# Kernel optimization log

Measured on AMD Instinct MI355X. Metric: run time of the kernel, lower is better.

Reference implementation:

```python
import jax, jax.numpy as jnp
import numpy as np

N_NODES = 50000
N_EDGES = 800000
FEAT = 128
HID1 = 128
HID2 = 64


def setup_inputs() -> dict:
    key = jax.random.key(0)
    k = jax.random.split(key, 6)
    x = jax.random.normal(k[0], (N_NODES, FEAT), dtype=jnp.float32)
    edge_index = jax.random.randint(k[1], (2, N_EDGES), 0, N_NODES, dtype=jnp.int32)
    # Glorot-style init scaling like PyG's GCNConv linear
    W1 = jax.random.normal(k[2], (FEAT, HID1), dtype=jnp.float32) * (1.0 / np.sqrt(FEAT))
    b1 = jnp.zeros((HID1,), dtype=jnp.float32)
    W2 = jax.random.normal(k[3], (HID1, HID2), dtype=jnp.float32) * (1.0 / np.sqrt(HID1))
    b2 = jnp.zeros((HID2,), dtype=jnp.float32)
    return {"x": x, "edge_index": edge_index, "W1": W1, "b1": b1, "W2": W2, "b2": b2}


def _gcn_conv(x, src, dst, W, b, n_nodes):
    """PyG GCNConv: h = X W; out_i = sum_j norm_ij h_j + b, with self-loops and
    symmetric normalization norm_ij = deg_i^-1/2 * deg_j^-1/2 (deg counts self-loop)."""
    h = x @ W  # [N, out]
    # degree at target nodes (self-loops already appended to src/dst)
    deg = jax.ops.segment_sum(jnp.ones_like(dst, dtype=h.dtype), dst, num_segments=n_nodes)
    dinv = jax.lax.rsqrt(jnp.maximum(deg, 1.0))  # deg >= 1 because of self-loops
    norm = dinv[src] * dinv[dst]  # [E+N]
    msg = h[src] * norm[:, None]  # gather + scale, [E+N, out]
    out = jax.ops.segment_sum(msg, dst, num_segments=n_nodes)
    return out + b


def reference(x, edge_index, W1, b1, W2, b2):
    n = x.shape[0]
    self_idx = jnp.arange(n, dtype=edge_index.dtype)
    src = jnp.concatenate([edge_index[0], self_idx])
    dst = jnp.concatenate([edge_index[1], self_idx])
    h = jax.nn.relu(_gcn_conv(x, src, dst, W1, b1, n))
    out = _gcn_conv(h, src, dst, W2, b2, n)
    return out
```

## Files before the change

### kernel.cpp

```cpp
#include <hip/hip_runtime.h>
#include <hip/hip_bf16.h>


#define POISON 0xAAAAAAAAu

typedef __attribute__((ext_vector_type(8))) short short8;
typedef __attribute__((ext_vector_type(4))) float f32x4;

__device__ __forceinline__ float bf_lo(unsigned u) { return __uint_as_float(u << 16); }
__device__ __forceinline__ float bf_hi(unsigned u) { return __uint_as_float(u & 0xffff0000u); }
__device__ __forceinline__ unsigned short f2bf(float f) {
    return (unsigned short)(__bfloat16_as_ushort(__float2bfloat16(f)));
}

__global__ __launch_bounds__(256) void countpack_kernel(
    const int* __restrict__ dst, unsigned* __restrict__ ucnt,
    int* __restrict__ eslot, int E,
    const float* __restrict__ W1, unsigned short* __restrict__ Wp1,
    const float* __restrict__ W2, unsigned short* __restrict__ Wp2) {
    constexpr int PB = (128 * 128 + 128 * 64) / 256;
    if ((int)blockIdx.x < PB) {
        int q = blockIdx.x * 256 + threadIdx.x;
        if (q < 128 * 128) {
            int j = q & 7;
            int n = (q >> 3) & 127;
            int kb = q >> 10;
            Wp1[q] = f2bf(W1[(kb * 8 + j) * 128 + n]);
        } else {
            int p = q - 128 * 128;
            int j = p & 7;
            int n = (p >> 3) & 63;
            int kb = p >> 9;
            Wp2[p] = f2bf(W2[(kb * 8 + j) * 64 + n]);
        }
        return;
    }
    int e = (blockIdx.x - PB) * 256 + threadIdx.x;
    if (e < E) eslot[e] = (int)(atomicAdd(&ucnt[dst[e]], 1u) - POISON);
}

__global__ __launch_bounds__(256) void alloc_kernel(unsigned* __restrict__ ucnt,
                                                    int* __restrict__ row_ptr,
                                                    float* __restrict__ dinv, int N) {
    int i = blockIdx.x * 256 + threadIdx.x;
    int lane = threadIdx.x & 63;
    int c = (i < N) ? (int)(ucnt[i] - POISON) : 0;
    if (i < N) dinv[i] = rsqrtf((float)(c + 1));
    int incl = c;
#pragma unroll
    for (int off = 1; off < 64; off <<= 1) {
        int u = __shfl_up(incl, off, 64);
        if (lane >= off) incl += u;
    }
    int base = 0;
    if (lane == 63) base = (int)(atomicAdd(&ucnt[N], (unsigned)incl) - POISON);
    base = __shfl(base, 63, 64);
    if (i < N) row_ptr[i] = base + incl - c;
}

__global__ __launch_bounds__(256) void scatgemm_kernel(
    const int* __restrict__ src, const int* __restrict__ dst,
    const int* __restrict__ row_ptr, const int* __restrict__ eslot,
    int* __restrict__ ssrc, int E,
    const float* __restrict__ X, const unsigned short* __restrict__ Wp1,
    const float* __restrict__ dinv, unsigned short* __restrict__ g1,
    int N, int gb) {
    if ((int)blockIdx.x >= gb) {
        int e0 = (blockIdx.x - gb) * 1024 + threadIdx.x * 4;
        if (e0 + 3 < E) {
            int4 d4 = *(const int4*)(dst + e0);
            int4 s4 = *(const int4*)(src + e0);
            int4 t4 = *(const int4*)(eslot + e0);
            ssrc[row_ptr[d4.x] + t4.x] = s4.x;
            ssrc[row_ptr[d4.y] + t4.y] = s4.y;
            ssrc[row_ptr[d4.z] + t4.z] = s4.z;
            ssrc[row_ptr[d4.w] + t4.w] = s4.w;
        } else {
            for (int e = e0; e < E; ++e)
                ssrc[row_ptr[dst[e]] + eslot[e]] = src[e];
        }
        return;
    }
    constexpr int NT = 8;
    const int lane = threadIdx.x & 63;
    const int wave = threadIdx.x >> 6;
    const int col = lane & 15;
    const int quad = lane >> 4;
    const int row0w = (blockIdx.x * 4 + wave) * 16;

    int arow = row0w + col;
    if (arow >= N) arow = N - 1;

    short8 afr[4];
    const float* Xr = X + (size_t)arow * 128;
#pragma unroll
    for (int c = 0; c < 4; ++c) {
        float4 f0 = *(const float4*)(Xr + c * 32 + quad * 8);
        float4 f1 = *(const float4*)(Xr + c * 32 + quad * 8 + 4);
        short8 a;
        a[0] = (short)f2bf(f0.x); a[1] = (short)f2bf(f0.y);
        a[2] = (short)f2bf(f0.z); a[3] = (short)f2bf(f0.w);
        a[4] = (short)f2bf(f1.x); a[5] = (short)f2bf(f1.y);
        a[6] = (short)f2bf(f1.z); a[7] = (short)f2bf(f1.w);
        afr[c] = a;
    }

    f32x4 acc[NT];
#pragma unroll
    for (int t = 0; t < NT; ++t) acc[t] = (f32x4){0.f, 0.f, 0.f, 0.f};

    const uint4* Wq = (const uint4*)Wp1;
#pragma unroll
    for (int c = 0; c < 4; ++c) {
        short8 bfr[NT];
#pragma unroll
        for (int t = 0; t < NT; ++t) {
            union { uint4 u; short8 s; } cv;
            cv.u = Wq[(size_t)(c * 4 + quad) * 128 + t * 16 + col];
            bfr[t] = cv.s;
        }
#pragma unroll
        for (int t = 0; t < NT; ++t)
            acc[t] = __builtin_amdgcn_mfma_f32_16x16x32_bf16(afr[c], bfr[t], acc[t], 0, 0, 0);
    }

#pragma unroll
    for (int r = 0; r < 4; ++r) {
        int row = row0w + quad * 4 + r;
        if (row < N) {
            float dv = dinv[row];
#pragma unroll
            for (int t = 0; t < NT; ++t)
                g1[(size_t)row * 128 + t * 16 + col] = f2bf(acc[t][r] * dv);
        }
    }
}

__global__ __launch_bounds__(256) void aggmm_kernel(const unsigned short* __restrict__ g1,
                                                    const int* __restrict__ row_ptr,
                                                    const unsigned* __restrict__ ucnt,
                                                    const int* __restrict__ ssrc,
                                                    const float* __restrict__ dinv,
                                                    const float* __restrict__ b1,
                                                    const unsigned short* __restrict__ Wp2,
                                                    unsigned short* __restrict__ g2, int N) {
    __shared__ unsigned short zt[16][136];
    __shared__ float sdinv[16];
    const int lane = threadIdx.x & 63;
    const int wave = threadIdx.x >> 6;
    const int nodebase = blockIdx.x * 16;
    const unsigned* hp = (const unsigned*)g1;

    const float bx = b1[2 * lane];
    const float by = b1[2 * lane + 1];

#pragma unroll
    for (int k = 0; k < 4; ++k) {
        int zr = wave * 4 + k;
        int node = __builtin_amdgcn_readfirstlane(nodebase + zr);
        unsigned pk = 0;
        if (node < N) {
            float di = dinv[node];
            int beg = row_ptr[node];
            int end = beg + (int)(ucnt[node] - POISON);
            unsigned hv = hp[node * 64 + lane];
            float ax0 = bf_lo(hv), ay0 = bf_hi(hv);
            float ax1 = 0.f, ay1 = 0.f;
            int j = beg;
            for (; j + 7 < end; j += 8) {
                int s0 = ssrc[j + 0], s1 = ssrc[j + 1], s2 = ssrc[j + 2], s3 = ssrc[j + 3];
                int s4 = ssrc[j + 4], s5 = ssrc[j + 5], s6 = ssrc[j + 6], s7 = ssrc[j + 7];
                unsigned v0 = hp[s0 * 64 + lane], v1 = hp[s1 * 64 + lane];
                unsigned v2 = hp[s2 * 64 + lane], v3 = hp[s3 * 64 + lane];
                unsigned v4 = hp[s4 * 64 + lane], v5 = hp[s5 * 64 + lane];
                unsigned v6 = hp[s6 * 64 + lane], v7 = hp[s7 * 64 + lane];
                ax0 += bf_lo(v0) + bf_lo(v1) + bf_lo(v2) + bf_lo(v3);
                ax1 += bf_lo(v4) + bf_lo(v5) + bf_lo(v6) + bf_lo(v7);
                ay0 += bf_hi(v0) + bf_hi(v1) + bf_hi(v2) + bf_hi(v3);
                ay1 += bf_hi(v4) + bf_hi(v5) + bf_hi(v6) + bf_hi(v7);
            }
            for (; j + 3 < end; j += 4) {
                int s0 = ssrc[j + 0], s1 = ssrc[j + 1], s2 = ssrc[j + 2], s3 = ssrc[j + 3];
                unsigned v0 = hp[s0 * 64 + lane], v1 = hp[s1 * 64 + lane];
                unsigned v2 = hp[s2 * 64 + lane], v3 = hp[s3 * 64 + lane];
                ax0 += bf_lo(v0) + bf_lo(v1);
                ax1 += bf_lo(v2) + bf_lo(v3);
                ay0 += bf_hi(v0) + bf_hi(v1);
                ay1 += bf_hi(v2) + bf_hi(v3);
            }
            for (; j < end; ++j) {
                unsigned v = hp[ssrc[j] * 64 + lane];
                ax0 += bf_lo(v);
                ay0 += bf_hi(v);
            }
            float ax = fmaxf((ax0 + ax1) * di + bx, 0.f);
            float ay = fmaxf((ay0 + ay1) * di + by, 0.f);
            pk = (unsigned)f2bf(ax) | ((unsigned)f2bf(ay) << 16);
            if (lane == 0) sdinv[zr] = di;
        } else if (lane == 0) {
            sdinv[zr] = 0.f;
        }
        ((unsigned*)&zt[zr][0])[lane] = pk;
    }
    __syncthreads();

    const int col = lane & 15;
    const int quad = lane >> 4;
    short8 afr[4];
#pragma unroll
    for (int c = 0; c < 4; ++c) {
        union { uint4 u; short8 s; } cv;
        cv.u = *(const uint4*)&zt[col][c * 32 + quad * 8];
        afr[c] = cv.s;
    }
    f32x4 acc = (f32x4){0.f, 0.f, 0.f, 0.f};
    const uint4* Wq = (const uint4*)Wp2;
#pragma unroll
    for (int c = 0; c < 4; ++c) {
        union { uint4 u; short8 s; } cv;
        cv.u = Wq[(size_t)(c * 4 + quad) * 64 + wave * 16 + col];
        acc = __builtin_amdgcn_mfma_f32_16x16x32_bf16(afr[c], cv.s, acc, 0, 0, 0);
    }
#pragma unroll
    for (int r = 0; r < 4; ++r) {
        int row = nodebase + quad * 4 + r;
        if (row < N)
            g2[(size_t)row * 64 + wave * 16 + col] = f2bf(acc[r] * sdinv[quad * 4 + r]);
    }
}

__global__ __launch_bounds__(256) void agg2_kernel(const unsigned short* __restrict__ g,
                                                   const int* __restrict__ row_ptr,
                                                   const unsigned* __restrict__ ucnt,
                                                   const int* __restrict__ ssrc,
                                                   const float* __restrict__ dinv,
                                                   const float* __restrict__ bias,
                                                   float* __restrict__ out, int N) {
    int node = __builtin_amdgcn_readfirstlane((int)(blockIdx.x * 4 + (threadIdx.x >> 6)));
    if (node >= N) return;
    int lane = threadIdx.x & 63;
    float di = dinv[node];
    int beg = row_ptr[node];
    int end = beg + (int)(ucnt[node] - POISON);

    float a0 = __uint_as_float((unsigned)g[node * 64 + lane] << 16);
    float a1 = 0.f;
    int j = beg;
    for (; j + 7 < end; j += 8) {
        int s0 = ssrc[j + 0], s1 = ssrc[j + 1], s2 = ssrc[j + 2], s3 = ssrc[j + 3];
        int s4 = ssrc[j + 4], s5 = ssrc[j + 5], s6 = ssrc[j + 6], s7 = ssrc[j + 7];
        float v0 = __uint_as_float((unsigned)g[s0 * 64 + lane] << 16);
        float v1 = __uint_as_float((unsigned)g[s1 * 64 + lane] << 16);
        float v2 = __uint_as_float((unsigned)g[s2 * 64 + lane] << 16);
        float v3 = __uint_as_float((unsigned)g[s3 * 64 + lane] << 16);
        float v4 = __uint_as_float((unsigned)g[s4 * 64 + lane] << 16);
        float v5 = __uint_as_float((unsigned)g[s5 * 64 + lane] << 16);
        float v6 = __uint_as_float((unsigned)g[s6 * 64 + lane] << 16);
        float v7 = __uint_as_float((unsigned)g[s7 * 64 + lane] << 16);
        a0 += v0 + v1 + v2 + v3;
        a1 += v4 + v5 + v6 + v7;
    }
    for (; j + 3 < end; j += 4) {
        int s0 = ssrc[j + 0], s1 = ssrc[j + 1], s2 = ssrc[j + 2], s3 = ssrc[j + 3];
        float v0 = __uint_as_float((unsigned)g[s0 * 64 + lane] << 16);
        float v1 = __uint_as_float((unsigned)g[s1 * 64 + lane] << 16);
        float v2 = __uint_as_float((unsigned)g[s2 * 64 + lane] << 16);
        float v3 = __uint_as_float((unsigned)g[s3 * 64 + lane] << 16);
        a0 += v0 + v1;
        a1 += v2 + v3;
    }
    for (; j < end; ++j)
        a0 += __uint_as_float((unsigned)g[ssrc[j] * 64 + lane] << 16);
    out[node * 64 + lane] = (a0 + a1) * di + bias[lane];
}

extern "C" void kernel_launch(void* const* d_in, const int* in_sizes, int n_in,
                              void* d_out, int out_size, void* d_ws, size_t ws_size,
                              hipStream_t stream) {
    const float* x = (const float*)d_in[0];
    const int* eidx = (const int*)d_in[1];
    const float* W1 = (const float*)d_in[2];
    const float* b1 = (const float*)d_in[3];
    const float* W2 = (const float*)d_in[4];
    const float* b2 = (const float*)d_in[5];
    float* out = (float*)d_out;

    const int N = in_sizes[0] / 128;
    const int E = in_sizes[1] / 2;
    const int* src = eidx;
    const int* dst = eidx + E;

    char* ws = (char*)d_ws;
    size_t off = 0;
    auto alloc = [&](size_t bytes) -> char* {
        char* p = ws + off;
        off = (off + bytes + 255) & ~(size_t)255;
        return p;
    };
    unsigned* ucnt = (unsigned*)alloc((size_t)(N + 1) * 4);
    int* row_ptr = (int*)alloc((size_t)N * 4);
    int* eslot = (int*)alloc((size_t)E * 4);
    int* ssrc = (int*)alloc((size_t)E * 4);
    float* dinv = (float*)alloc((size_t)N * 4);
    unsigned short* Wp1 = (unsigned short*)alloc(128 * 128 * 2);
    unsigned short* Wp2 = (unsigned short*)alloc(128 * 64 * 2);
    unsigned short* g1 = (unsigned short*)alloc((size_t)N * 128 * 2);
    unsigned short* g2 = (unsigned short*)alloc((size_t)N * 64 * 2);

    const int nbN = (N + 255) / 256;
    const int nbE = (E + 255) / 256;
    const int nbE4 = (E + 1023) / 1024;
    const int gb = (N + 63) / 64;
    constexpr int PB = (128 * 128 + 128 * 64) / 256;

    countpack_kernel<<<PB + nbE, 256, 0, stream>>>(dst, ucnt, eslot, E, W1, Wp1, W2, Wp2);
    alloc_kernel<<<nbN, 256, 0, stream>>>(ucnt, row_ptr, dinv, N);
    scatgemm_kernel<<<gb + nbE4, 256, 0, stream>>>(src, dst, row_ptr, eslot, ssrc, E,
                                                   x, Wp1, dinv, g1, N, gb);
    aggmm_kernel<<<(N + 15) / 16, 256, 0, stream>>>(g1, row_ptr, ucnt, ssrc, dinv, b1, Wp2, g2, N);
    agg2_kernel<<<(N + 3) / 4, 256, 0, stream>>>(g2, row_ptr, ucnt, ssrc, dinv, b2, out, N);
}
```

Measured before the change: 196.3 us.

## Split wave into half-wave node gathers with 8-byte loads and vectorize degree counting

The layer-1 aggregation now gives each half-wave (32 lanes) its own node, and every lane gathers 8 bytes (four bf16 features) per neighbor instead of 4. Two nodes are processed in parallel per wave, which is meant to raise memory-level parallelism on the irregular gather and cut per-node loop overhead. The degree-counting kernel now handles four edges per thread with int4 loads and stores, using a quarter of the blocks. In exchange, the aggregation unroll drops from 8 to 4, and the two half-waves can diverge when their nodes have different degrees.

```diff
diff --git a/kernel.cpp b/kernel.cpp
--- a/kernel.cpp
+++ b/kernel.cpp
@@ -35,8 +35,19 @@
         }
         return;
     }
-    int e = (blockIdx.x - PB) * 256 + threadIdx.x;
-    if (e < E) eslot[e] = (int)(atomicAdd(&ucnt[dst[e]], 1u) - POISON);
+    int e0 = (blockIdx.x - PB) * 1024 + threadIdx.x * 4;
+    if (e0 + 3 < E) {
+        int4 d4 = *(const int4*)(dst + e0);
+        int4 t;
+        t.x = (int)(atomicAdd(&ucnt[d4.x], 1u) - POISON);
+        t.y = (int)(atomicAdd(&ucnt[d4.y], 1u) - POISON);
+        t.z = (int)(atomicAdd(&ucnt[d4.z], 1u) - POISON);
+        t.w = (int)(atomicAdd(&ucnt[d4.w], 1u) - POISON);
+        *(int4*)(eslot + e0) = t;
+    } else {
+        for (int e = e0; e < E; ++e)
+            eslot[e] = (int)(atomicAdd(&ucnt[dst[e]], 1u) - POISON);
+    }
 }
 
 __global__ __launch_bounds__(256) void alloc_kernel(unsigned* __restrict__ ucnt,
@@ -148,59 +159,60 @@
     __shared__ float sdinv[16];
     const int lane = threadIdx.x & 63;
     const int wave = threadIdx.x >> 6;
+    const int h = lane >> 5;
+    const int u = lane & 31;
     const int nodebase = blockIdx.x * 16;
-    const unsigned* hp = (const unsigned*)g1;
-
-    const float bx = b1[2 * lane];
-    const float by = b1[2 * lane + 1];
-
-#pragma unroll
-    for (int k = 0; k < 4; ++k) {
-        int zr = wave * 4 + k;
-        int node = __builtin_amdgcn_readfirstlane(nodebase + zr);
-        unsigned pk = 0;
-        if (node < N) {
-            float di = dinv[node];
-            int beg = row_ptr[node];
-            int end = beg + (int)(ucnt[node] - POISON);
-            unsigned hv = hp[node * 64 + lane];
-            float ax0 = bf_lo(hv), ay0 = bf_hi(hv);
-            float ax1 = 0.f, ay1 = 0.f;
-            int j = beg;
-            for (; j + 7 < end; j += 8) {
-                int s0 = ssrc[j + 0], s1 = ssrc[j + 1], s2 = ssrc[j + 2], s3 = ssrc[j + 3];
-                int s4 = ssrc[j + 4], s5 = ssrc[j + 5], s6 = ssrc[j + 6], s7 = ssrc[j + 7];
-                unsigned v0 = hp[s0 * 64 + lane], v1 = hp[s1 * 64 + lane];
-                unsigned v2 = hp[s2 * 64 + lane], v3 = hp[s3 * 64 + lane];
-                unsigned v4 = hp[s4 * 64 + lane], v5 = hp[s5 * 64 + lane];
-                unsigned v6 = hp[s6 * 64 + lane], v7 = hp[s7 * 64 + lane];
-                ax0 += bf_lo(v0) + bf_lo(v1) + bf_lo(v2) + bf_lo(v3);
-                ax1 += bf_lo(v4) + bf_lo(v5) + bf_lo(v6) + bf_lo(v7);
-                ay0 += bf_hi(v0) + bf_hi(v1) + bf_hi(v2) + bf_hi(v3);
-                ay1 += bf_hi(v4) + bf_hi(v5) + bf_hi(v6) + bf_hi(v7);
-            }
-            for (; j + 3 < end; j += 4) {
-                int s0 = ssrc[j + 0], s1 = ssrc[j + 1], s2 = ssrc[j + 2], s3 = ssrc[j + 3];
-                unsigned v0 = hp[s0 * 64 + lane], v1 = hp[s1 * 64 + lane];
-                unsigned v2 = hp[s2 * 64 + lane], v3 = hp[s3 * 64 + lane];
-                ax0 += bf_lo(v0) + bf_lo(v1);
-                ax1 += bf_lo(v2) + bf_lo(v3);
-                ay0 += bf_hi(v0) + bf_hi(v1);
-                ay1 += bf_hi(v2) + bf_hi(v3);
-            }
-            for (; j < end; ++j) {
-                unsigned v = hp[ssrc[j] * 64 + lane];
-                ax0 += bf_lo(v);
-                ay0 += bf_hi(v);
-            }
-            float ax = fmaxf((ax0 + ax1) * di + bx, 0.f);
-            float ay = fmaxf((ay0 + ay1) * di + by, 0.f);
-            pk = (unsigned)f2bf(ax) | ((unsigned)f2bf(ay) << 16);
-            if (lane == 0) sdinv[zr] = di;
-        } else if (lane == 0) {
-            sdinv[zr] = 0.f;
-        }
-        ((unsigned*)&zt[zr][0])[lane] = pk;
+    const uint2* hp2 = (const uint2*)g1;
+
+    const float4 b4 = *(const float4*)(b1 + 4 * u);
+
+#pragma unroll
+    for (int k = 0; k < 2; ++k) {
+        int zr = wave * 4 + k * 2 + h;
+        int node = nodebase + zr;
+        bool act = node < N;
+        float di = 0.f;
+        int beg = 0, deg = 0;
+        uint2 hv = {0u, 0u};
+        if (act) {
+            di = dinv[node];
+            beg = row_ptr[node];
+            deg = (int)(ucnt[node] - POISON);
+            hv = hp2[(size_t)node * 32 + u];
+        }
+        float a0 = 0.f, a1 = 0.f, a2 = 0.f, a3 = 0.f;
+        int j = 0;
+        for (; j + 4 <= deg; j += 4) {
+            int s0 = ssrc[beg + j + 0], s1 = ssrc[beg + j + 1];
+            int s2 = ssrc[beg + j + 2], s3 = ssrc[beg + j + 3];
+            uint2 v0 = hp2[(size_t)s0 * 32 + u];
+            uint2 v1 = hp2[(size_t)s1 * 32 + u];
+            uint2 v2 = hp2[(size_t)s2 * 32 + u];
+            uint2 v3 = hp2[(size_t)s3 * 32 + u];
+            a0 += bf_lo(v0.x) + bf_lo(v1.x) + bf_lo(v2.x) + bf_lo(v3.x);
+            a1 += bf_hi(v0.x) + bf_hi(v1.x) + bf_hi(v2.x) + bf_hi(v3.x);
+            a2 += bf_lo(v0.y) + bf_lo(v1.y) + bf_lo(v2.y) + bf_lo(v3.y);
+            a3 += bf_hi(v0.y) + bf_hi(v1.y) + bf_hi(v2.y) + bf_hi(v3.y);
+        }
+        for (; j < deg; ++j) {
+            int s = ssrc[beg + j];
+            uint2 v = hp2[(size_t)s * 32 + u];
+            a0 += bf_lo(v.x); a1 += bf_hi(v.x);
+            a2 += bf_lo(v.y); a3 += bf_hi(v.y);
+        }
+        uint2 pk = {0u, 0u};
+        if (act) {
+            a0 += bf_lo(hv.x); a1 += bf_hi(hv.x);
+            a2 += bf_lo(hv.y); a3 += bf_hi(hv.y);
+            float z0 = fmaxf(a0 * di + b4.x, 0.f);
+            float z1 = fmaxf(a1 * di + b4.y, 0.f);
+            float z2 = fmaxf(a2 * di + b4.z, 0.f);
+            float z3 = fmaxf(a3 * di + b4.w, 0.f);
+            pk.x = (unsigned)f2bf(z0) | ((unsigned)f2bf(z1) << 16);
+            pk.y = (unsigned)f2bf(z2) | ((unsigned)f2bf(z3) << 16);
+        }
+        *(uint2*)&zt[zr][4 * u] = pk;
+        if (u == 0) sdinv[zr] = act ? di : 0.f;
     }
     __syncthreads();
 
@@ -209,16 +221,16 @@
     short8 afr[4];
 #pragma unroll
     for (int c = 0; c < 4; ++c) {
-        union { uint4 u; short8 s; } cv;
-        cv.u = *(const uint4*)&zt[col][c * 32 + quad * 8];
+        union { uint4 u4; short8 s; } cv;
+        cv.u4 = *(const uint4*)&zt[col][c * 32 + quad * 8];
         afr[c] = cv.s;
     }
     f32x4 acc = (f32x4){0.f, 0.f, 0.f, 0.f};
     const uint4* Wq = (const uint4*)Wp2;
 #pragma unroll
     for (int c = 0; c < 4; ++c) {
-        union { uint4 u; short8 s; } cv;
-        cv.u = Wq[(size_t)(c * 4 + quad) * 64 + wave * 16 + col];
+        union { uint4 u4; short8 s; } cv;
+        cv.u4 = Wq[(size_t)(c * 4 + quad) * 64 + wave * 16 + col];
         acc = __builtin_amdgcn_mfma_f32_16x16x32_bf16(afr[c], cv.s, acc, 0, 0, 0);
     }
 #pragma unroll
@@ -308,12 +320,11 @@
     unsigned short* g2 = (unsigned short*)alloc((size_t)N * 64 * 2);
 
     const int nbN = (N + 255) / 256;
-    const int nbE = (E + 255) / 256;
     const int nbE4 = (E + 1023) / 1024;
     const int gb = (N + 63) / 64;
     constexpr int PB = (128 * 128 + 128 * 64) / 256;
 
-    countpack_kernel<<<PB + nbE, 256, 0, stream>>>(dst, ucnt, eslot, E, W1, Wp1, W2, Wp2);
+    countpack_kernel<<<PB + nbE4, 256, 0, stream>>>(dst, ucnt, eslot, E, W1, Wp1, W2, Wp2);
     alloc_kernel<<<nbN, 256, 0, stream>>>(ucnt, row_ptr, dinv, N);
     scatgemm_kernel<<<gb + nbE4, 256, 0, stream>>>(src, dst, row_ptr, eslot, ssrc, E,
                                                    x, Wp1, dinv, g1, N, gb);
```

Measured after the change: 202.2 us. +3.0%, slower.
